# Optimization experiments

Measured on AMD Instinct MI355X. Metric: run time of the kernel, lower is better.

Reference implementation:

```python
import jax, jax.numpy as jnp
import numpy as np

N, DEG = 20000, 16          # nodes, fixed neighbor-list length
H, C, D, IN = 4, 16, 128, 256  # cluster_heads, num_centroids, hidden_dim, input_dim
NEG_SLOPE = 0.2


def setup_inputs() -> dict:
    key = jax.random.key(0)
    ks = jax.random.split(key, 12)
    s_in = 1.0 / np.sqrt(IN)
    s_h = 1.0 / np.sqrt(D)
    inp = {
        "x_node": jax.random.normal(ks[0], (N, IN), dtype=jnp.float32),
        "adj": jax.random.randint(ks[1], (N, DEG), 0, N, dtype=jnp.int32),
        "epoch": 1,
        # linear layers (torch convention: W [out, in])
        "W1": jax.random.uniform(ks[2], (D, IN), jnp.float32, -s_in, s_in),
        "b1": jax.random.uniform(ks[3], (D,), jnp.float32, -s_in, s_in),
        "W2": jax.random.uniform(ks[4], (D, D), jnp.float32, -s_h, s_h),
        "b2": jax.random.uniform(ks[5], (D,), jnp.float32, -s_h, s_h),
        "W21": jax.random.uniform(ks[6], (D, D), jnp.float32, -s_h, s_h),
        "b21": jax.random.uniform(ks[7], (D,), jnp.float32, -s_h, s_h),
        # centroids: 2*rand-1, shape [H, C*D]
        "centroids": 2.0 * jax.random.uniform(ks[8], (H, C * D), dtype=jnp.float32) - 1.0,
        # headConv: xavier_uniform gain=1.414 on [H, 1]
        "headConv": jax.random.uniform(ks[9], (H, 1), jnp.float32,
                                       -1.414 * np.sqrt(6.0 / (H + 1)),
                                       1.414 * np.sqrt(6.0 / (H + 1))),
    }
    return inp


def _leaky(x):
    return jnp.where(x >= 0, x, NEG_SLOPE * x)


def _cluster_block(h, adj, centroids, headConv):
    # h: [N, D]; adj: [N, deg]; centroids: [H, C*D]; headConv: [H, 1]
    cent = centroids.reshape(H, C, D)
    # squared L2 distance dist[h,c,n] = ||x_n - cent_hc||^2 (norm expansion,
    # avoids the [H,C,N,D] broadcast the torch code materializes)
    hn2 = jnp.sum(h * h, axis=-1)                      # [N]
    cn2 = jnp.sum(cent * cent, axis=-1)                # [H, C]
    cross = jnp.einsum('hcd,nd->hcn', cent, h)         # [H, C, N]
    dist = cn2[..., None] + hn2[None, None, :] - 2.0 * cross
    # nu=1: q = (1 + dist)^-1
    q = 1.0 / (1.0 + dist)                             # [H, C, N]
    # gather neighbor scores per node and normalize over the edge dim
    qn = q[:, :, adj]                                  # [H, C, N, deg]
    qn = qn / jnp.sum(qn, axis=3, keepdims=True)
    # combine heads with headConv, then softmax over edges per centroid
    w = jnp.einsum('hcne,h->nce', qn, headConv[:, 0])  # [N, C, deg]
    w = jax.nn.softmax(w, axis=2)
    # weighted aggregation of neighbor features
    new_feat = jnp.einsum('nce,ned->ncd', w, h[adj])   # [N, C, D]
    return new_feat


def reference(x_node, adj, epoch, W1, b1, W2, b2, W21, b21, centroids, headConv):
    # eval mode: dropout is identity
    x = _leaky(x_node @ W1.T + b1)
    h_prime = _leaky(x @ W2.T + b2)                    # [N, D]
    new_feat = _cluster_block(h_prime, adj, centroids, headConv)
    new_feat = _leaky(new_feat @ W21.T + b21)          # [N, C, D]
    return (h_prime, new_feat)
```

## Files before the change

### kernel.cpp

```cpp
#include <hip/hip_runtime.h>
#include <cstdint>
#include <cstddef>

#define NEG_SLOPE 0.2f

typedef __attribute__((ext_vector_type(8))) short bf16x8;
typedef __attribute__((ext_vector_type(8))) unsigned short u16x8;
typedef __attribute__((ext_vector_type(4))) float f32x4;

__device__ __forceinline__ float leaky_f(float x) { return x >= 0.f ? x : NEG_SLOPE * x; }

__device__ __forceinline__ unsigned short f2bf(float f) {
    union { float f; uint32_t u; } v; v.f = f;
    return (unsigned short)((v.u + 0x7fffu + ((v.u >> 16) & 1u)) >> 16);
}
__device__ __forceinline__ float bf2f(unsigned short u) {
    union { uint32_t u; float f; } v; v.u = ((uint32_t)u) << 16; return v.f;
}
__device__ __forceinline__ float bfhi(uint32_t w) {
    union { uint32_t u; float f; } v; v.u = w & 0xffff0000u; return v.f;
}
__device__ __forceinline__ float bflo(uint32_t w) {
    union { uint32_t u; float f; } v; v.u = w << 16; return v.f;
}
__device__ __forceinline__ u16x8 cvt8(float4 a, float4 b) {
    u16x8 o;
    o[0] = f2bf(a.x); o[1] = f2bf(a.y); o[2] = f2bf(a.z); o[3] = f2bf(a.w);
    o[4] = f2bf(b.x); o[5] = f2bf(b.y); o[6] = f2bf(b.z); o[7] = f2bf(b.w);
    return o;
}

__global__ __launch_bounds__(256)
void pack_kernel(const float* __restrict__ x_node, const float* __restrict__ W1,
                 const float* __restrict__ W2, const float* __restrict__ W21,
                 const float* __restrict__ cent,
                 unsigned short* __restrict__ xb, unsigned short* __restrict__ pw1,
                 unsigned short* __restrict__ pw2, unsigned short* __restrict__ pw3,
                 float* __restrict__ cn2g, int N)
{
    const int bid = blockIdx.x, tid = threadIdx.x;
    if (bid < 36) {
        const int sub = tid >> 6, lane = tid & 63, g = bid * 4 + sub;
        const int l15 = lane & 15, l4 = lane >> 4;
        const float* src; unsigned short* dst;
        if (g < 64) {
            int step = g >> 3, f = g & 7;
            src = W1 + (size_t)(f * 16 + l15) * 256 + step * 32 + l4 * 8;
            dst = pw1 + ((size_t)(step * 8 + f) * 64 + lane) * 8;
        } else if (g < 96) {
            int gg = g - 64, step = gg >> 3, f = gg & 7;
            src = W2 + (size_t)(f * 16 + l15) * 128 + step * 32 + l4 * 8;
            dst = pw2 + ((size_t)(step * 8 + f) * 64 + lane) * 8;
        } else {
            int gg = g - 96, step = gg / 12, f = gg % 12;
            int brow = f * 16 + l15;
            const float* base = (brow < 128) ? (W21 + (size_t)brow * 128)
                                             : (cent + (size_t)(brow - 128) * 128);
            src = base + step * 32 + l4 * 8;
            dst = pw3 + ((size_t)(step * 12 + f) * 64 + lane) * 8;
        }
        float4 a = *reinterpret_cast<const float4*>(src);
        float4 b = *reinterpret_cast<const float4*>(src + 4);
        *reinterpret_cast<u16x8*>(dst) = cvt8(a, b);
    } else if (bid == 36) {
        int r = tid >> 2, c0 = (tid & 3) * 32;
        const float* cr = cent + (size_t)r * 128 + c0;
        float s = 0.f;
#pragma unroll
        for (int q = 0; q < 8; q++) {
            float4 v = *reinterpret_cast<const float4*>(cr + q * 4);
            s += v.x * v.x + v.y * v.y + v.z * v.z + v.w * v.w;
        }
        s += __shfl_xor(s, 1); s += __shfl_xor(s, 2);
        if ((tid & 3) == 0) cn2g[r] = s;
    } else {
        size_t base = (size_t)(bid - 37) * 4096 + (size_t)tid * 16;
        float4 v0 = *reinterpret_cast<const float4*>(x_node + base);
        float4 v1 = *reinterpret_cast<const float4*>(x_node + base + 4);
        float4 v2 = *reinterpret_cast<const float4*>(x_node + base + 8);
        float4 v3 = *reinterpret_cast<const float4*>(x_node + base + 12);
        *reinterpret_cast<u16x8*>(xb + base)     = cvt8(v0, v1);
        *reinterpret_cast<u16x8*>(xb + base + 8) = cvt8(v2, v3);
    }
}

__global__ __launch_bounds__(256)
void fused_gemms(const unsigned short* __restrict__ xb,
                 const unsigned short* __restrict__ pw1, const unsigned short* __restrict__ pw2,
                 const unsigned short* __restrict__ pw3,
                 const float* __restrict__ b1, const float* __restrict__ b2,
                 const float* __restrict__ cn2g,
                 float* __restrict__ h_out, unsigned short* __restrict__ hWb,
                 unsigned short* __restrict__ qtb, int N)
{
    __shared__ __align__(16) short Xs[16 * 136];
    __shared__ float hn2s[4][16];

    const int tid = threadIdx.x, wave = tid >> 6, lane = tid & 63;
    const int l15 = lane & 15, l4 = lane >> 4;
    const int rowBlk = blockIdx.x * 16;

    f32x4 a0{0.f,0.f,0.f,0.f}, a1{0.f,0.f,0.f,0.f}, a2{0.f,0.f,0.f,0.f};
    {
        const unsigned short* ap = xb + (size_t)(rowBlk + l15) * 256 + l4 * 8;
        const unsigned short* bp = pw1 + (size_t)(wave * 2) * 512 + lane * 8;
#pragma unroll
        for (int k = 0; k < 8; k++) {
            bf16x8 af = *reinterpret_cast<const bf16x8*>(ap + k * 32);
            bf16x8 bf0 = *reinterpret_cast<const bf16x8*>(bp + (size_t)k * 8 * 512);
            bf16x8 bf1 = *reinterpret_cast<const bf16x8*>(bp + (size_t)k * 8 * 512 + 512);
            a0 = __builtin_amdgcn_mfma_f32_16x16x32_bf16(af, bf0, a0, 0, 0, 0);
            a1 = __builtin_amdgcn_mfma_f32_16x16x32_bf16(af, bf1, a1, 0, 0, 0);
        }
        float bia = b1[wave * 32 + l15], bib = b1[wave * 32 + 16 + l15];
#pragma unroll
        for (int j = 0; j < 4; j++) {
            Xs[(l4 * 4 + j) * 136 + wave * 32 + l15]      = (short)f2bf(leaky_f(a0[j] + bia));
            Xs[(l4 * 4 + j) * 136 + wave * 32 + 16 + l15] = (short)f2bf(leaky_f(a1[j] + bib));
        }
    }
    __syncthreads();

    a0 = f32x4{0.f,0.f,0.f,0.f}; a1 = f32x4{0.f,0.f,0.f,0.f};
    const short* xp = &Xs[l15 * 136 + l4 * 8];
    {
        const unsigned short* bp = pw2 + (size_t)(wave * 2) * 512 + lane * 8;
#pragma unroll
        for (int k = 0; k < 4; k++) {
            bf16x8 af = *reinterpret_cast<const bf16x8*>(xp + k * 32);
            bf16x8 bf0 = *reinterpret_cast<const bf16x8*>(bp + (size_t)k * 8 * 512);
            bf16x8 bf1 = *reinterpret_cast<const bf16x8*>(bp + (size_t)k * 8 * 512 + 512);
            a0 = __builtin_amdgcn_mfma_f32_16x16x32_bf16(af, bf0, a0, 0, 0, 0);
            a1 = __builtin_amdgcn_mfma_f32_16x16x32_bf16(af, bf1, a1, 0, 0, 0);
        }
    }
    float hv0[4], hv1[4], pn[4];
    {
        float bia = b2[wave * 32 + l15], bib = b2[wave * 32 + 16 + l15];
#pragma unroll
        for (int j = 0; j < 4; j++) {
            hv0[j] = leaky_f(a0[j] + bia);
            hv1[j] = leaky_f(a1[j] + bib);
            float s = hv0[j] * hv0[j] + hv1[j] * hv1[j];
            s += __shfl_xor(s, 1); s += __shfl_xor(s, 2);
            s += __shfl_xor(s, 4); s += __shfl_xor(s, 8);
            pn[j] = s;
        }
    }
    __syncthreads();
#pragma unroll
    for (int j = 0; j < 4; j++) {
        int gr = rowBlk + l4 * 4 + j;
        __builtin_nontemporal_store(hv0[j], &h_out[(size_t)gr * 128 + wave * 32 + l15]);
        __builtin_nontemporal_store(hv1[j], &h_out[(size_t)gr * 128 + wave * 32 + 16 + l15]);
        Xs[(l4 * 4 + j) * 136 + wave * 32 + l15]      = (short)f2bf(hv0[j]);
        Xs[(l4 * 4 + j) * 136 + wave * 32 + 16 + l15] = (short)f2bf(hv1[j]);
        if (l15 == 0) hn2s[wave][l4 * 4 + j] = pn[j];
    }
    __syncthreads();

    a0 = f32x4{0.f,0.f,0.f,0.f}; a1 = f32x4{0.f,0.f,0.f,0.f}; a2 = f32x4{0.f,0.f,0.f,0.f};
    {
        const unsigned short* bp = pw3 + (size_t)(wave * 3) * 512 + lane * 8;
#pragma unroll
        for (int k = 0; k < 4; k++) {
            bf16x8 af = *reinterpret_cast<const bf16x8*>(xp + k * 32);
            bf16x8 bf0 = *reinterpret_cast<const bf16x8*>(bp + (size_t)k * 12 * 512);
            bf16x8 bf1 = *reinterpret_cast<const bf16x8*>(bp + (size_t)k * 12 * 512 + 512);
            bf16x8 bf2 = *reinterpret_cast<const bf16x8*>(bp + (size_t)k * 12 * 512 + 1024);
            a0 = __builtin_amdgcn_mfma_f32_16x16x32_bf16(af, bf0, a0, 0, 0, 0);
            a1 = __builtin_amdgcn_mfma_f32_16x16x32_bf16(af, bf1, a1, 0, 0, 0);
            a2 = __builtin_amdgcn_mfma_f32_16x16x32_bf16(af, bf2, a2, 0, 0, 0);
        }
    }
    {
        float hn2r[4];
#pragma unroll
        for (int j = 0; j < 4; j++)
            hn2r[j] = hn2s[0][l4 * 4 + j] + hn2s[1][l4 * 4 + j]
                    + hn2s[2][l4 * 4 + j] + hn2s[3][l4 * 4 + j];
        f32x4 av[3] = {a0, a1, a2};
#pragma unroll
        for (int ff = 0; ff < 3; ff++) {
            int col = wave * 48 + ff * 16 + l15;
            if (col < 128) {
#pragma unroll
                for (int j = 0; j < 4; j++) {
                    int gr = rowBlk + l4 * 4 + j;
                    hWb[(size_t)gr * 128 + col] = f2bf(av[ff][j]);
                }
            } else {
                int c2 = col - 128;
                float cn2v = cn2g[c2];
#pragma unroll
                for (int j = 0; j < 4; j++) {
                    int gr = rowBlk + l4 * 4 + j;
                    float q = 1.f / (1.f + cn2v + hn2r[j] - 2.f * av[ff][j]);
                    qtb[(size_t)gr * 64 + c2] = f2bf(q);
                }
            }
        }
    }
}

__global__ __launch_bounds__(256)
void agg_kernel(const int* __restrict__ adj, const unsigned short* __restrict__ qtb,
                const unsigned short* __restrict__ hWb, const float* __restrict__ b21,
                const float* __restrict__ headConv, float* __restrict__ out1)
{
    __shared__ __align__(16) unsigned short qs[4][16 * 64];
    __shared__ __align__(16) unsigned short hs[4][16 * 128];
    __shared__ float wbuf[4][16][16];

    const int wv = threadIdx.x >> 6, lane = threadIdx.x & 63;
    const int n = blockIdx.x * 4 + wv;

    int myadj = adj[n * 16 + (lane & 15)];

#pragma unroll
    for (int i = 0; i < 2; i++) {
        int row = i * 8 + (lane >> 3);
        int nb = __shfl(myadj, row);
        *reinterpret_cast<u16x8*>(&qs[wv][i * 512 + lane * 8]) =
            *reinterpret_cast<const u16x8*>(qtb + (size_t)nb * 64 + (lane & 7) * 8);
    }
#pragma unroll
    for (int i = 0; i < 4; i++) {
        int row = i * 4 + (lane >> 4);
        int nb = __shfl(myadj, row);
        *reinterpret_cast<u16x8*>(&hs[wv][i * 512 + lane * 8]) =
            *reinterpret_cast<const u16x8*>(hWb + (size_t)nb * 128 + (lane & 15) * 8);
    }
    __syncthreads();

    {
        float qv[16];
        float s = 0.f;
#pragma unroll
        for (int e = 0; e < 16; e++) { qv[e] = bf2f(qs[wv][e * 64 + lane]); s += qv[e]; }
        float rs = 1.f / s;
        float conv = headConv[lane >> 4];
        float wn[16], m = -1e30f;
#pragma unroll
        for (int e = 0; e < 16; e++) {
            float t = conv * qv[e] * rs;
            t += __shfl_xor(t, 16);
            t += __shfl_xor(t, 32);
            wn[e] = t;
            m = fmaxf(m, t);
        }
        float sum = 0.f;
#pragma unroll
        for (int e = 0; e < 16; e++) { wn[e] = __expf(wn[e] - m); sum += wn[e]; }
        float inv = 1.f / sum;
        const int c = lane & 15, eg = lane >> 4;
#pragma unroll
        for (int j = 0; j < 4; j++) wbuf[wv][eg * 4 + j][c] = wn[eg * 4 + j] * inv;
    }
    __syncthreads();

    {
        const int dg = lane & 15, cg = lane >> 4, d0 = dg * 4;
        float bv[8];
        *reinterpret_cast<float4*>(bv)     = *reinterpret_cast<const float4*>(b21 + d0);
        *reinterpret_cast<float4*>(bv + 4) = *reinterpret_cast<const float4*>(b21 + d0 + 64);
        float acc[4][8];
#pragma unroll
        for (int jc = 0; jc < 4; jc++)
#pragma unroll
            for (int j = 0; j < 8; j++) acc[jc][j] = bv[j];

#pragma unroll
        for (int e = 0; e < 16; e++) {
            uint2 wlo = *reinterpret_cast<const uint2*>(&hs[wv][e * 128 + d0]);
            uint2 whi = *reinterpret_cast<const uint2*>(&hs[wv][e * 128 + 64 + d0]);
            float hv[8];
            hv[0] = bflo(wlo.x); hv[1] = bfhi(wlo.x); hv[2] = bflo(wlo.y); hv[3] = bfhi(wlo.y);
            hv[4] = bflo(whi.x); hv[5] = bfhi(whi.x); hv[6] = bflo(whi.y); hv[7] = bfhi(whi.y);
#pragma unroll
            for (int jc = 0; jc < 4; jc++) {
                float w = wbuf[wv][e][cg * 4 + jc];
#pragma unroll
                for (int j = 0; j < 8; j++) acc[jc][j] = fmaf(w, hv[j], acc[jc][j]);
            }
        }
#pragma unroll
        for (int jc = 0; jc < 4; jc++) {
            f32x4 lo, hi;
#pragma unroll
            for (int j = 0; j < 4; j++) { lo[j] = leaky_f(acc[jc][j]); hi[j] = leaky_f(acc[jc][j + 4]); }
            float* dst = out1 + ((size_t)(n * 16 + cg * 4 + jc)) * 128;
            __builtin_nontemporal_store(lo, reinterpret_cast<f32x4*>(dst + d0));
            __builtin_nontemporal_store(hi, reinterpret_cast<f32x4*>(dst + d0 + 64));
        }
    }
}

extern "C" void kernel_launch(void* const* d_in, const int* in_sizes, int n_in,
                              void* d_out, int out_size, void* d_ws, size_t ws_size,
                              hipStream_t stream)
{
    const float* x_node   = (const float*)d_in[0];
    const int*   adj      = (const int*)  d_in[1];
    const float* W1       = (const float*)d_in[3];
    const float* b1       = (const float*)d_in[4];
    const float* W2       = (const float*)d_in[5];
    const float* b2       = (const float*)d_in[6];
    const float* W21      = (const float*)d_in[7];
    const float* b21      = (const float*)d_in[8];
    const float* cent     = (const float*)d_in[9];
    const float* headConv = (const float*)d_in[10];

    const int N = in_sizes[0] / 256;

    float* h    = (float*)d_out;
    float* out1 = h + (size_t)N * 128;

    unsigned short* xb  = (unsigned short*)d_ws;
    unsigned short* hWb = xb  + (size_t)N * 256;
    unsigned short* qtb = hWb + (size_t)N * 128;
    unsigned short* pw1 = qtb + (size_t)N * 64;
    unsigned short* pw2 = pw1 + 32768;
    unsigned short* pw3 = pw2 + 16384;
    float*          cn2g = (float*)(pw3 + 24576);

    const int xblocks = (N * 256) / 4096;

    pack_kernel<<<37 + xblocks, 256, 0, stream>>>(x_node, W1, W2, W21, cent,
                                                  xb, pw1, pw2, pw3, cn2g, N);
    fused_gemms<<<N / 16, 256, 0, stream>>>(xb, pw1, pw2, pw3, b1, b2, cn2g,
                                            h, hWb, qtb, N);
    agg_kernel<<<N / 4, 256, 0, stream>>>(adj, qtb, hWb, b21, headConv, out1);
}
```

Measured before the change: 68.58 us.

## Fuse x_node bf16 conversion into GEMM and use MFMA for aggregation

New measurement: 75.28 us. +9.8%, slower.

```diff
diff --git a/kernel.cpp b/kernel.cpp
--- a/kernel.cpp
+++ b/kernel.cpp
@@ -5,6 +5,7 @@
 #define NEG_SLOPE 0.2f
 
 typedef __attribute__((ext_vector_type(8))) short bf16x8;
+typedef __attribute__((ext_vector_type(4))) short s16x4;
 typedef __attribute__((ext_vector_type(8))) unsigned short u16x8;
 typedef __attribute__((ext_vector_type(4))) float f32x4;
 
@@ -16,12 +17,6 @@
 }
 __device__ __forceinline__ float bf2f(unsigned short u) {
     union { uint32_t u; float f; } v; v.u = ((uint32_t)u) << 16; return v.f;
-}
-__device__ __forceinline__ float bfhi(uint32_t w) {
-    union { uint32_t u; float f; } v; v.u = w & 0xffff0000u; return v.f;
-}
-__device__ __forceinline__ float bflo(uint32_t w) {
-    union { uint32_t u; float f; } v; v.u = w << 16; return v.f;
 }
 __device__ __forceinline__ u16x8 cvt8(float4 a, float4 b) {
     u16x8 o;
@@ -31,12 +26,10 @@
 }
 
 __global__ __launch_bounds__(256)
-void pack_kernel(const float* __restrict__ x_node, const float* __restrict__ W1,
-                 const float* __restrict__ W2, const float* __restrict__ W21,
-                 const float* __restrict__ cent,
-                 unsigned short* __restrict__ xb, unsigned short* __restrict__ pw1,
-                 unsigned short* __restrict__ pw2, unsigned short* __restrict__ pw3,
-                 float* __restrict__ cn2g, int N)
+void pack_kernel(const float* __restrict__ W1, const float* __restrict__ W2,
+                 const float* __restrict__ W21, const float* __restrict__ cent,
+                 unsigned short* __restrict__ pw1, unsigned short* __restrict__ pw2,
+                 unsigned short* __restrict__ pw3, float* __restrict__ cn2g)
 {
     const int bid = blockIdx.x, tid = threadIdx.x;
     if (bid < 36) {
@@ -62,7 +55,7 @@
         float4 a = *reinterpret_cast<const float4*>(src);
         float4 b = *reinterpret_cast<const float4*>(src + 4);
         *reinterpret_cast<u16x8*>(dst) = cvt8(a, b);
-    } else if (bid == 36) {
+    } else {
         int r = tid >> 2, c0 = (tid & 3) * 32;
         const float* cr = cent + (size_t)r * 128 + c0;
         float s = 0.f;
@@ -73,19 +66,11 @@
         }
         s += __shfl_xor(s, 1); s += __shfl_xor(s, 2);
         if ((tid & 3) == 0) cn2g[r] = s;
-    } else {
-        size_t base = (size_t)(bid - 37) * 4096 + (size_t)tid * 16;
-        float4 v0 = *reinterpret_cast<const float4*>(x_node + base);
-        float4 v1 = *reinterpret_cast<const float4*>(x_node + base + 4);
-        float4 v2 = *reinterpret_cast<const float4*>(x_node + base + 8);
-        float4 v3 = *reinterpret_cast<const float4*>(x_node + base + 12);
-        *reinterpret_cast<u16x8*>(xb + base)     = cvt8(v0, v1);
-        *reinterpret_cast<u16x8*>(xb + base + 8) = cvt8(v2, v3);
     }
 }
 
 __global__ __launch_bounds__(256)
-void fused_gemms(const unsigned short* __restrict__ xb,
+void fused_gemms(const float* __restrict__ x_node,
                  const unsigned short* __restrict__ pw1, const unsigned short* __restrict__ pw2,
                  const unsigned short* __restrict__ pw3,
                  const float* __restrict__ b1, const float* __restrict__ b2,
@@ -93,6 +78,7 @@
                  float* __restrict__ h_out, unsigned short* __restrict__ hWb,
                  unsigned short* __restrict__ qtb, int N)
 {
+    __shared__ __align__(16) short As[16 * 264];
     __shared__ __align__(16) short Xs[16 * 136];
     __shared__ float hn2s[4][16];
 
@@ -100,9 +86,21 @@
     const int l15 = lane & 15, l4 = lane >> 4;
     const int rowBlk = blockIdx.x * 16;
 
+    {
+        int r = tid >> 4, c0 = (tid & 15) * 16;
+        const float* src = x_node + (size_t)(rowBlk + r) * 256 + c0;
+        float4 v0 = *reinterpret_cast<const float4*>(src);
+        float4 v1 = *reinterpret_cast<const float4*>(src + 4);
+        float4 v2 = *reinterpret_cast<const float4*>(src + 8);
+        float4 v3 = *reinterpret_cast<const float4*>(src + 12);
+        *reinterpret_cast<u16x8*>(&As[r * 264 + c0])     = cvt8(v0, v1);
+        *reinterpret_cast<u16x8*>(&As[r * 264 + c0 + 8]) = cvt8(v2, v3);
+    }
+    __syncthreads();
+
     f32x4 a0{0.f,0.f,0.f,0.f}, a1{0.f,0.f,0.f,0.f}, a2{0.f,0.f,0.f,0.f};
     {
-        const unsigned short* ap = xb + (size_t)(rowBlk + l15) * 256 + l4 * 8;
+        const short* ap = &As[l15 * 264 + l4 * 8];
         const unsigned short* bp = pw1 + (size_t)(wave * 2) * 512 + lane * 8;
 #pragma unroll
         for (int k = 0; k < 8; k++) {
@@ -208,14 +206,21 @@
                 const unsigned short* __restrict__ hWb, const float* __restrict__ b21,
                 const float* __restrict__ headConv, float* __restrict__ out1)
 {
-    __shared__ __align__(16) unsigned short qs[4][16 * 64];
-    __shared__ __align__(16) unsigned short hs[4][16 * 128];
-    __shared__ float wbuf[4][16][16];
-
-    const int wv = threadIdx.x >> 6, lane = threadIdx.x & 63;
+    __shared__ __align__(16) unsigned short qs[4][1024];
+    __shared__ __align__(16) unsigned short hs[4][2048];
+    __shared__ __align__(16) unsigned short zb[64];
+
+    const int tid = threadIdx.x;
+    const int wv = tid >> 6, lane = tid & 63;
+    const int eg = lane >> 4, l15 = lane & 15;
     const int n = blockIdx.x * 4 + wv;
 
-    int myadj = adj[n * 16 + (lane & 15)];
+    if (tid < 8) {
+        u16x8 z{};
+        *reinterpret_cast<u16x8*>(&zb[tid * 8]) = z;
+    }
+
+    int myadj = adj[n * 16 + l15];
 
 #pragma unroll
     for (int i = 0; i < 2; i++) {
@@ -224,22 +229,31 @@
         *reinterpret_cast<u16x8*>(&qs[wv][i * 512 + lane * 8]) =
             *reinterpret_cast<const u16x8*>(qtb + (size_t)nb * 64 + (lane & 7) * 8);
     }
-#pragma unroll
-    for (int i = 0; i < 4; i++) {
-        int row = i * 4 + (lane >> 4);
-        int nb = __shfl(myadj, row);
-        *reinterpret_cast<u16x8*>(&hs[wv][i * 512 + lane * 8]) =
-            *reinterpret_cast<const u16x8*>(hWb + (size_t)nb * 128 + (lane & 15) * 8);
-    }
-    __syncthreads();
-
+
+    {
+        const int equad = (eg & 1) * 2 + (l15 >> 3);
+        const int e_st  = equad * 4 + ((l15 >> 1) & 3);
+        const int nb    = __shfl(myadj, e_st);
+        const int inner = ((l15 >> 1) & 3) * 32 + (l15 & 1) * 16;
+#pragma unroll
+        for (int i = 0; i < 4; i++) {
+            int db  = i * 2 + (eg >> 1);
+            int oct = db * 2 + (l15 & 1);
+            int byteoff = (db * 4 + equad) * 128 + inner;
+            *reinterpret_cast<u16x8*>(&hs[wv][byteoff >> 1]) =
+                *reinterpret_cast<const u16x8*>(hWb + (size_t)nb * 128 + oct * 8);
+        }
+    }
+    __syncthreads();
+
+    bf16x8 afrag;
     {
         float qv[16];
         float s = 0.f;
 #pragma unroll
         for (int e = 0; e < 16; e++) { qv[e] = bf2f(qs[wv][e * 64 + lane]); s += qv[e]; }
         float rs = 1.f / s;
-        float conv = headConv[lane >> 4];
+        float conv = headConv[eg];
         float wn[16], m = -1e30f;
 #pragma unroll
         for (int e = 0; e < 16; e++) {
@@ -253,45 +267,58 @@
 #pragma unroll
         for (int e = 0; e < 16; e++) { wn[e] = __expf(wn[e] - m); sum += wn[e]; }
         float inv = 1.f / sum;
-        const int c = lane & 15, eg = lane >> 4;
-#pragma unroll
-        for (int j = 0; j < 4; j++) wbuf[wv][eg * 4 + j][c] = wn[eg * 4 + j] * inv;
-    }
-    __syncthreads();
-
-    {
-        const int dg = lane & 15, cg = lane >> 4, d0 = dg * 4;
-        float bv[8];
-        *reinterpret_cast<float4*>(bv)     = *reinterpret_cast<const float4*>(b21 + d0);
-        *reinterpret_cast<float4*>(bv + 4) = *reinterpret_cast<const float4*>(b21 + d0 + 64);
-        float acc[4][8];
-#pragma unroll
-        for (int jc = 0; jc < 4; jc++)
-#pragma unroll
-            for (int j = 0; j < 8; j++) acc[jc][j] = bv[j];
-
-#pragma unroll
-        for (int e = 0; e < 16; e++) {
-            uint2 wlo = *reinterpret_cast<const uint2*>(&hs[wv][e * 128 + d0]);
-            uint2 whi = *reinterpret_cast<const uint2*>(&hs[wv][e * 128 + 64 + d0]);
-            float hv[8];
-            hv[0] = bflo(wlo.x); hv[1] = bfhi(wlo.x); hv[2] = bflo(wlo.y); hv[3] = bfhi(wlo.y);
-            hv[4] = bflo(whi.x); hv[5] = bfhi(whi.x); hv[6] = bflo(whi.y); hv[7] = bfhi(whi.y);
-#pragma unroll
-            for (int jc = 0; jc < 4; jc++) {
-                float w = wbuf[wv][e][cg * 4 + jc];
-#pragma unroll
-                for (int j = 0; j < 8; j++) acc[jc][j] = fmaf(w, hv[j], acc[jc][j]);
+        bf16x8 w0{}, w1{}, wz{};
+#pragma unroll
+        for (int j = 0; j < 8; j++) {
+            w0[j] = (short)f2bf(wn[j] * inv);
+            w1[j] = (short)f2bf(wn[8 + j] * inv);
+        }
+        afrag = (eg == 0) ? w0 : (eg == 1) ? w1 : wz;
+    }
+
+    s16x4 tr[16];
+    {
+        uint32_t rb  = (uint32_t)(uintptr_t)&hs[wv][0];
+        uint32_t zba = (uint32_t)(uintptr_t)&zb[0];
+        uint32_t base = (eg < 2) ? (rb + (uint32_t)(eg * 256 + l15 * 8))
+                                 : (zba + (uint32_t)(l15 * 8));
+        uint32_t step = (eg < 2) ? 512u : 0u;
+        uint32_t d1   = (eg < 2) ? 128u : 0u;
+#pragma unroll
+        for (int db = 0; db < 8; db++) {
+            uint32_t a0 = base + (uint32_t)db * step;
+            uint32_t a1 = a0 + d1;
+            asm volatile("ds_read_b64_tr_b16 %0, %1" : "=&v"(tr[2 * db])     : "v"(a0));
+            asm volatile("ds_read_b64_tr_b16 %0, %1" : "=&v"(tr[2 * db + 1]) : "v"(a1));
+        }
+        asm volatile("s_waitcnt lgkmcnt(0)" ::: "memory");
+        __builtin_amdgcn_sched_barrier(0);
+    }
+
+    f32x4 facc[8];
+#pragma unroll
+    for (int db = 0; db < 8; db++) {
+        bf16x8 bfrag;
+        s16x4 ra = tr[2 * db], rb2 = tr[2 * db + 1];
+        bfrag[0] = ra[0]; bfrag[1] = ra[1]; bfrag[2] = ra[2]; bfrag[3] = ra[3];
+        bfrag[4] = rb2[0]; bfrag[5] = rb2[1]; bfrag[6] = rb2[2]; bfrag[7] = rb2[3];
+        f32x4 z{0.f, 0.f, 0.f, 0.f};
+        facc[db] = __builtin_amdgcn_mfma_f32_16x16x32_bf16(afrag, bfrag, z, 0, 0, 0);
+    }
+
+    {
+        float bb[8];
+#pragma unroll
+        for (int db = 0; db < 8; db++) bb[db] = b21[db * 16 + l15];
+        float* obase = out1 + ((size_t)n * 16 + eg * 4) * 128 + l15;
+#pragma unroll
+        for (int jj = 0; jj < 4; jj++) {
+            float* orow = obase + (size_t)jj * 128;
+#pragma unroll
+            for (int db = 0; db < 8; db++) {
+                float v = leaky_f(facc[db][jj] + bb[db]);
+                __builtin_nontemporal_store(v, orow + db * 16);
             }
-        }
-#pragma unroll
-        for (int jc = 0; jc < 4; jc++) {
-            f32x4 lo, hi;
-#pragma unroll
-            for (int j = 0; j < 4; j++) { lo[j] = leaky_f(acc[jc][j]); hi[j] = leaky_f(acc[jc][j + 4]); }
-            float* dst = out1 + ((size_t)(n * 16 + cg * 4 + jc)) * 128;
-            __builtin_nontemporal_store(lo, reinterpret_cast<f32x4*>(dst + d0));
-            __builtin_nontemporal_store(hi, reinterpret_cast<f32x4*>(dst + d0 + 64));
         }
     }
 }
@@ -316,19 +343,15 @@
     float* h    = (float*)d_out;
     float* out1 = h + (size_t)N * 128;
 
-    unsigned short* xb  = (unsigned short*)d_ws;
-    unsigned short* hWb = xb  + (size_t)N * 256;
+    unsigned short* hWb = (unsigned short*)d_ws;
     unsigned short* qtb = hWb + (size_t)N * 128;
     unsigned short* pw1 = qtb + (size_t)N * 64;
     unsigned short* pw2 = pw1 + 32768;
     unsigned short* pw3 = pw2 + 16384;
     float*          cn2g = (float*)(pw3 + 24576);
 
-    const int xblocks = (N * 256) / 4096;
-
-    pack_kernel<<<37 + xblocks, 256, 0, stream>>>(x_node, W1, W2, W21, cent,
-                                                  xb, pw1, pw2, pw3, cn2g, N);
-    fused_gemms<<<N / 16, 256, 0, stream>>>(xb, pw1, pw2, pw3, b1, b2, cn2g,
+    pack_kernel<<<37, 256, 0, stream>>>(W1, W2, W21, cent, pw1, pw2, pw3, cn2g);
+    fused_gemms<<<N / 16, 256, 0, stream>>>(x_node, pw1, pw2, pw3, b1, b2, cn2g,
                                             h, hWb, qtb, N);
     agg_kernel<<<N / 4, 256, 0, stream>>>(adj, qtb, hWb, b21, headConv, out1);
 }
```
